# Performance work log

Measured on AMD Instinct MI355X. Metric: run time of the kernel, lower is better.

The kernel has to match this reference:

```python
import jax, jax.numpy as jnp
import numpy as np

NUM_HEADS = 16
HEAD_SIZE = 128


def _alibi_mask(seq_len: int, num_heads: int) -> jnp.ndarray:
    # slopes: num_heads > 8 branch -> 1 / 2**(i/2)
    if num_heads <= 8:
        slopes = jnp.asarray([1.0 / 2.0 ** i for i in range(num_heads)], dtype=jnp.float32)
    else:
        slopes = jnp.asarray([1.0 / 2.0 ** (i / 2.0) for i in range(num_heads)], dtype=jnp.float32)
    i = jnp.arange(seq_len)[:, None]
    j = jnp.arange(seq_len)[None, :]
    # -(i-j) on/below diagonal, -inf strictly above (causal)
    base = jnp.where(j <= i, -(i - j).astype(jnp.float32), -jnp.inf)  # [S, S]
    return slopes[:, None, None] * base  # [H, S, S]; slope * -inf = -inf


def setup_inputs() -> dict:
    key = jax.random.key(0)
    ks = jax.random.split(key, 5)
    H = 2048
    s = 0.02
    return {
        "x": jax.random.normal(ks[0], (2, 2048, H), dtype=jnp.float32),
        "qkv_w": jax.random.normal(ks[1], (H, 3 * NUM_HEADS * HEAD_SIZE), dtype=jnp.float32) * s,
        "qkv_b": jax.random.normal(ks[2], (3 * NUM_HEADS * HEAD_SIZE,), dtype=jnp.float32) * s,
        "out_w": jax.random.normal(ks[3], (NUM_HEADS * HEAD_SIZE, H), dtype=jnp.float32) * s,
        "out_b": jax.random.normal(ks[4], (H,), dtype=jnp.float32) * s,
    }


def reference(x, qkv_w, qkv_b, out_w, out_b):
    b, s, h = x.shape
    qkv = x @ qkv_w + qkv_b  # [b, s, 3*H*D]
    q, k, v = jnp.split(qkv, 3, axis=-1)

    def to_heads(t):
        return t.reshape(b, s, NUM_HEADS, HEAD_SIZE).transpose(0, 2, 1, 3)  # [b,h,s,d]

    q, k, v = to_heads(q), to_heads(k), to_heads(v)
    # NOTE: original module does NOT scale by 1/sqrt(d)
    scores = jnp.einsum("bhid,bhjd->bhij", q, k) + _alibi_mask(s, NUM_HEADS)[None]
    attn = jax.nn.softmax(scores, axis=-1)
    ctx = jnp.einsum("bhij,bhjd->bhid", attn, v)  # [b,h,s,d]
    ctx = ctx.transpose(0, 2, 1, 3).reshape(b, s, NUM_HEADS * HEAD_SIZE)
    return ctx @ out_w + out_b
```

## Files before the change

### kernel.cpp

```cpp
#include <hip/hip_runtime.h>

typedef _Float16 h8 __attribute__((ext_vector_type(8)));
typedef _Float16 h4 __attribute__((ext_vector_type(4)));
typedef float f4 __attribute__((ext_vector_type(4)));

#define MFMA16(a, b, c) __builtin_amdgcn_mfma_f32_16x16x32_f16((a), (b), (c), 0, 0, 0)
#define AS1 __attribute__((address_space(1)))
#define AS3 __attribute__((address_space(3)))

static __device__ __forceinline__ void load_lds16(const _Float16* g, _Float16* l) {
  __builtin_amdgcn_global_load_lds((const AS1 void*)g, (AS3 void*)l, 16, 0, 0);
}

__global__ __launch_bounds__(256) void cvt_f32_f16(const float* __restrict__ in,
                                                   _Float16* __restrict__ out, int n) {
  int i = (blockIdx.x * 256 + threadIdx.x) * 4;
  if (i < n) {
    const float4 v = *(const float4*)(in + i);
    h4 o;
    o[0] = (_Float16)v.x; o[1] = (_Float16)v.y; o[2] = (_Float16)v.z; o[3] = (_Float16)v.w;
    *(h4*)(out + i) = o;
  }
}

__global__ __launch_bounds__(256) void transpose_cvt(const float* __restrict__ W,
                                                     _Float16* __restrict__ Wt, int K, int N) {
  __shared__ _Float16 t[64][66];
  int n0 = blockIdx.x * 64, k0 = blockIdx.y * 64;
  int c = threadIdx.x & 63, r0 = threadIdx.x >> 6;
  for (int i = 0; i < 16; i++) {
    int r = r0 * 16 + i;
    t[r][c] = (_Float16)W[(size_t)(k0 + r) * N + n0 + c];
  }
  __syncthreads();
  for (int i = 0; i < 16; i++) {
    int r = r0 * 16 + i;
    Wt[(size_t)(n0 + r) * K + k0 + c] = t[c][r];
  }
}

template <int MODE>
__global__ __launch_bounds__(512, 2) void gemm_bt(const _Float16* __restrict__ A,
                                                  const _Float16* __restrict__ Bt,
                                                  const float* __restrict__ bias, int K,
                                                  _Float16* __restrict__ qp,
                                                  _Float16* __restrict__ kp,
                                                  _Float16* __restrict__ vtp,
                                                  float* __restrict__ outp, int N) {
  __shared__ __align__(16) _Float16 LDS[3][24576];
  const int m0 = blockIdx.y * 128, n0 = blockIdx.x * 256;
  const int tid = threadIdx.x;
  const int w = tid >> 6, lane = tid & 63, quad = lane >> 4, l16 = lane & 15;
  const int wmo = (w >> 2) * 64, wno = (w & 3) * 64;
  const int qq = lane >> 3, bb = lane & 7;
  const int lc8 = (bb ^ qq) * 8;

  const _Float16* ap0 = A + (size_t)(m0 + w * 16 + qq) * K + lc8;
  const _Float16* bp0 = Bt + (size_t)(n0 + w * 32 + qq) * K + lc8;
  const int wA = w * 1024, wB = 8192 + w * 2048;

  f4 acc[4][4] = {};
  const int nk = K >> 6;

#define STAGE(slot, koff)                               \
  {                                                     \
    const _Float16* ap = ap0 + (koff);                  \
    const _Float16* bp = bp0 + (koff);                  \
    _Float16* la = &LDS[slot][wA];                      \
    _Float16* lb = &LDS[slot][wB];                      \
    load_lds16(ap, la);                                 \
    load_lds16(ap + (size_t)8 * K, la + 512);           \
    load_lds16(bp, lb);                                 \
    load_lds16(bp + (size_t)8 * K, lb + 512);           \
    load_lds16(bp + (size_t)16 * K, lb + 1024);         \
    load_lds16(bp + (size_t)24 * K, lb + 1536);         \
  }

  STAGE(0, 0);
  STAGE(1, 64);
  asm volatile("s_waitcnt vmcnt(6)" ::: "memory");
  __builtin_amdgcn_s_barrier();

  int cb = 0, sb = 2;
  for (int t = 0; t < nk; ++t) {
    if (t + 2 < nk) STAGE(sb, (t + 2) * 64);
    sb = cb;
    const _Float16* As = &LDS[cb][0];
    const _Float16* Bs = &LDS[cb][8192];
#pragma unroll
    for (int ks = 0; ks < 2; ks++) {
      h8 af[4], bf[4];
#pragma unroll
      for (int mi = 0; mi < 4; mi++) {
        const int r = wmo + mi * 16 + l16;
        const int pc = (ks * 4 + quad) ^ (l16 & 7);
        af[mi] = *(const h8*)(&As[r * 64 + pc * 8]);
      }
#pragma unroll
      for (int ni = 0; ni < 4; ni++) {
        const int r = wno + ni * 16 + l16;
        const int pc = (ks * 4 + quad) ^ (l16 & 7);
        bf[ni] = *(const h8*)(&Bs[r * 64 + pc * 8]);
      }
      __builtin_amdgcn_s_setprio(1);
#pragma unroll
      for (int mi = 0; mi < 4; mi++)
#pragma unroll
        for (int ni = 0; ni < 4; ni++) acc[mi][ni] = MFMA16(af[mi], bf[ni], acc[mi][ni]);
      __builtin_amdgcn_s_setprio(0);
    }
    if (t + 1 < nk) {
      if (t + 2 < nk)
        asm volatile("s_waitcnt vmcnt(6)" ::: "memory");
      else
        asm volatile("s_waitcnt vmcnt(0)" ::: "memory");
      __builtin_amdgcn_s_barrier();
    }
    cb = (cb == 2) ? 0 : cb + 1;
  }
#undef STAGE

  if constexpr (MODE == 0) {
    _Float16* U = &LDS[0][0];
    const int which = n0 >> 11;
    const int bq = m0 >> 11, ms = m0 & 2047;
    const int wn_ = w & 3;
    const int grp = wn_ >> 1, cl = (wn_ & 1) * 64;
    for (int g = 0; g < 2; ++g) {
      __syncthreads();
      if (grp == g) {
        if (which == 2) {
#pragma unroll
          for (int mi = 0; mi < 4; mi++)
#pragma unroll
            for (int ni = 0; ni < 4; ni++) {
              const int d = cl + ni * 16 + l16;
              const float bv = bias[n0 + g * 128 + d];
              const int s0 = wmo + mi * 16 + quad * 4;
              h4 pack;
#pragma unroll
              for (int r = 0; r < 4; r++) pack[r] = (_Float16)(acc[mi][ni][r] + bv);
              *(h4*)(&U[d * 136 + s0]) = pack;
            }
        } else {
#pragma unroll
          for (int mi = 0; mi < 4; mi++)
#pragma unroll
            for (int ni = 0; ni < 4; ni++) {
              const int d = cl + ni * 16 + l16;
              const float bv = bias[n0 + g * 128 + d];
#pragma unroll
              for (int r = 0; r < 4; r++) {
                const int s = wmo + mi * 16 + quad * 4 + r;
                U[s * 136 + d] = (_Float16)(acc[mi][ni][r] + bv);
              }
            }
        }
      }
      __syncthreads();
      const int hh = ((n0 + g * 128) >> 7) & 15;
      const size_t hb = (size_t)bq * 16 + hh;
      if (which == 2) {
        _Float16* dst = vtp + hb * (size_t)(128 * 2048) + ms;
#pragma unroll
        for (int i = 0; i < 4; i++) {
          int f = i * 512 + tid, row = f >> 4, ch = f & 15;
          *(h8*)(dst + (size_t)row * 2048 + ch * 8) = *(h8*)(&U[row * 136 + ch * 8]);
        }
      } else {
        _Float16* dst = (which == 0 ? qp : kp) + (hb * 2048 + ms) * (size_t)128;
#pragma unroll
        for (int i = 0; i < 4; i++) {
          int f = i * 512 + tid, row = f >> 4, ch = f & 15;
          *(h8*)(dst + (size_t)row * 128 + ch * 8) = *(h8*)(&U[row * 136 + ch * 8]);
        }
      }
    }
  } else {
#pragma unroll
    for (int mi = 0; mi < 4; mi++)
#pragma unroll
      for (int ni = 0; ni < 4; ni++) {
        const int gm = m0 + wmo + mi * 16 + quad * 4;
        const int gn = n0 + wno + ni * 16 + l16;
        const float bv = bias[gn];
#pragma unroll
        for (int r = 0; r < 4; r++) outp[(size_t)(gm + r) * N + gn] = acc[mi][ni][r] + bv;
      }
  }
}

__global__ __launch_bounds__(256, 2) void attn_kernel(const _Float16* __restrict__ Q,
                                                      const _Float16* __restrict__ Kg,
                                                      const _Float16* __restrict__ Vt,
                                                      _Float16* __restrict__ ctx) {
  __shared__ _Float16 Ks[2][8192];
  __shared__ _Float16 Vs[2][8192];
  __shared__ _Float16 Vones[1088];
  __shared__ _Float16 Pl[4][16 * 68];

  const int bh = blockIdx.x, px = blockIdx.y;
  const int b = bh >> 4, h = bh & 15;
  const int tid = threadIdx.x, w = tid >> 6, lane = tid & 63, quad = lane >> 4, l16 = lane & 15;
  const size_t hbo = (size_t)bh * (2048 * 128);
  const _Float16* Qh = Q + hbo;
  const _Float16* Kh = Kg + hbo;
  const _Float16* Vh = Vt + hbo;
  const float slope = exp2f(-0.5f * (float)h);
  const float L2E = 1.44269504088896f;
  const float NEG = -3.0e38f;

  for (int i = tid; i < 1088; i += 256) Vones[i] = (_Float16)0.f;
  if (tid < 64) Vones[tid] = (_Float16)1.f;

  float cj[4];
  for (int jf = 0; jf < 4; jf++) cj[jf] = slope * (float)(jf * 16 + l16);

  const int kle = (l16 ^ quad) * 8, klo = kle ^ 32;
  const int lq = lane >> 3, vlc = ((lane & 7) ^ lq) * 8;

  for (int phase = 0; phase < 2; phase++) {
    const int t = phase ? px : 31 - px;
    const int qbase = t * 64 + w * 16;

    h8 aq[4];
#pragma unroll
    for (int t4 = 0; t4 < 4; t4++)
      aq[t4] = *(const h8*)(Qh + (size_t)(qbase + l16) * 128 + t4 * 32 + quad * 8);

    f4 o[9] = {};
    float m_i[4];
    for (int r = 0; r < 4; r++) m_i[r] = NEG;

    const int jtiles = t + 1;
    __syncthreads();
    if (w < 2) {
      const _Float16* kb = Kh + (size_t)(32 * w + quad) * 128;
      _Float16* dst = &Ks[0][w * 4096];
#pragma unroll
      for (int cc = 0; cc < 8; cc++)
        load_lds16(kb + (size_t)(4 * cc) * 128 + ((cc & 1) ? klo : kle), dst + cc * 512);
    } else {
      const _Float16* vb = Vh + (size_t)(64 * (w - 2) + lq) * 2048 + vlc;
      _Float16* dst = &Vs[0][(w - 2) * 4096];
#pragma unroll
      for (int cc = 0; cc < 8; cc++) load_lds16(vb + (size_t)(8 * cc) * 2048, dst + cc * 512);
    }

    for (int jt = 0; jt < jtiles; jt++) {
      const int j0 = jt * 64, cur = jt & 1;
      __syncthreads();
      if (jt + 1 < jtiles) {
        const int nj0 = j0 + 64, nb = cur ^ 1;
        if (w < 2) {
          const _Float16* kb = Kh + (size_t)(nj0 + 32 * w + quad) * 128;
          _Float16* dst = &Ks[nb][w * 4096];
#pragma unroll
          for (int cc = 0; cc < 8; cc++)
            load_lds16(kb + (size_t)(4 * cc) * 128 + ((cc & 1) ? klo : kle), dst + cc * 512);
        } else {
          const _Float16* vb = Vh + (size_t)(64 * (w - 2) + lq) * 2048 + nj0 + vlc;
          _Float16* dst = &Vs[nb][(w - 2) * 4096];
#pragma unroll
          for (int cc = 0; cc < 8; cc++) load_lds16(vb + (size_t)(8 * cc) * 2048, dst + cc * 512);
        }
      }
      f4 sc[4] = {};
#pragma unroll
      for (int jf = 0; jf < 4; jf++) {
        const int row = jf * 16 + l16;
#pragma unroll
        for (int t4 = 0; t4 < 4; t4++) {
          const int p = (t4 * 4 + quad) ^ (l16 & 7);
          h8 bk = *(const h8*)(&Ks[cur][row * 128 + p * 8]);
          sc[jf] = MFMA16(aq[t4], bk, sc[jf]);
        }
      }
      const float bj0 = slope * (float)j0;
#pragma unroll
      for (int jf = 0; jf < 4; jf++) {
        const float cb = bj0 + cj[jf];
#pragma unroll
        for (int r = 0; r < 4; r++) sc[jf][r] += cb;
      }
      if (jt == jtiles - 1) {
#pragma unroll
        for (int jf = 0; jf < 4; jf++) {
          const int j = j0 + jf * 16 + l16;
#pragma unroll
          for (int r = 0; r < 4; r++)
            if (j > qbase + quad * 4 + r) sc[jf][r] = NEG;
        }
      }
      float m_new[4], alpha[4];
#pragma unroll
      for (int r = 0; r < 4; r++) {
        float v = fmaxf(fmaxf(sc[0][r], sc[1][r]), fmaxf(sc[2][r], sc[3][r]));
        v = fmaxf(v, __shfl_xor(v, 1));
        v = fmaxf(v, __shfl_xor(v, 2));
        v = fmaxf(v, __shfl_xor(v, 4));
        v = fmaxf(v, __shfl_xor(v, 8));
        m_new[r] = fmaxf(m_i[r], v);
        alpha[r] = exp2f((m_i[r] - m_new[r]) * L2E);
        m_i[r] = m_new[r];
      }
#pragma unroll
      for (int jf = 0; jf < 4; jf++)
#pragma unroll
        for (int r = 0; r < 4; r++) sc[jf][r] = exp2f((sc[jf][r] - m_new[r]) * L2E);
#pragma unroll
      for (int nt = 0; nt < 9; nt++)
#pragma unroll
        for (int r = 0; r < 4; r++) o[nt][r] *= alpha[r];
#pragma unroll
      for (int jf = 0; jf < 4; jf++)
#pragma unroll
        for (int r = 0; r < 4; r++)
          Pl[w][(quad * 4 + r) * 68 + jf * 16 + l16] = (_Float16)sc[jf][r];
      asm volatile("s_waitcnt lgkmcnt(0)" ::: "memory");
      h8 ap0 = *(const h8*)(&Pl[w][l16 * 68 + quad * 8]);
      h8 ap1 = *(const h8*)(&Pl[w][l16 * 68 + 32 + quad * 8]);
#pragma unroll
      for (int nt = 0; nt < 8; nt++) {
        const int row = nt * 16 + l16;
        const int p0 = quad ^ (l16 & 7), p1 = (4 + quad) ^ (l16 & 7);
        h8 bv0 = *(const h8*)(&Vs[cur][row * 64 + p0 * 8]);
        h8 bv1 = *(const h8*)(&Vs[cur][row * 64 + p1 * 8]);
        o[nt] = MFMA16(ap0, bv0, o[nt]);
        o[nt] = MFMA16(ap1, bv1, o[nt]);
      }
      {
        h8 b0 = *(const h8*)(&Vones[l16 * 68 + quad * 8]);
        h8 b1 = *(const h8*)(&Vones[l16 * 68 + 32 + quad * 8]);
        o[8] = MFMA16(ap0, b0, o[8]);
        o[8] = MFMA16(ap1, b1, o[8]);
      }
    }

#pragma unroll
    for (int r = 0; r < 4; r++) {
      float lsum = __shfl(o[8][r], lane & 48);
      float inv = 1.0f / lsum;
      const int i = qbase + quad * 4 + r;
      const size_t row = (size_t)b * 2048 + i;
#pragma unroll
      for (int nt = 0; nt < 8; nt++)
        ctx[row * 2048 + h * 128 + nt * 16 + l16] = (_Float16)(o[nt][r] * inv);
    }
  }
}

extern "C" void kernel_launch(void* const* d_in, const int* in_sizes, int n_in, void* d_out,
                              int out_size, void* d_ws, size_t ws_size, hipStream_t stream) {
  const float* x = (const float*)d_in[0];
  const float* qkv_w = (const float*)d_in[1];
  const float* qkv_b = (const float*)d_in[2];
  const float* out_w = (const float*)d_in[3];
  const float* out_b = (const float*)d_in[4];
  float* out = (float*)d_out;

  char* ws = (char*)d_ws;
  if (ws_size < 117440512u) return;
  _Float16* xb  = (_Float16*)(ws + 0);
  _Float16* wqt = (_Float16*)(ws + 16777216);
  _Float16* wot = (_Float16*)(ws + 41943040);
  _Float16* q   = (_Float16*)(ws + 50331648);
  _Float16* k   = (_Float16*)(ws + 67108864);
  _Float16* vt  = (_Float16*)(ws + 83886080);
  _Float16* ctx = (_Float16*)(ws + 100663296);

  cvt_f32_f16<<<8192, 256, 0, stream>>>(x, xb, 8388608);
  transpose_cvt<<<dim3(96, 32), 256, 0, stream>>>(qkv_w, wqt, 2048, 6144);
  transpose_cvt<<<dim3(32, 32), 256, 0, stream>>>(out_w, wot, 2048, 2048);
  gemm_bt<0><<<dim3(24, 32), 512, 0, stream>>>(xb, wqt, qkv_b, 2048, q, k, vt, nullptr, 6144);
  attn_kernel<<<dim3(32, 16), 256, 0, stream>>>(q, k, vt, ctx);
  gemm_bt<1><<<dim3(8, 32), 512, 0, stream>>>(ctx, wot, out_b, 2048, nullptr, nullptr, nullptr,
                                              out, 2048);
}
```

Before: 393.5 us.

## Restructure GEMM mainloop into two-buffer split-phase pipeline with staggered A/B loads

```diff
diff --git a/kernel.cpp b/kernel.cpp
--- a/kernel.cpp
+++ b/kernel.cpp
@@ -40,95 +40,122 @@
 }
 
 template <int MODE>
-__global__ __launch_bounds__(512, 2) void gemm_bt(const _Float16* __restrict__ A,
-                                                  const _Float16* __restrict__ Bt,
-                                                  const float* __restrict__ bias, int K,
-                                                  _Float16* __restrict__ qp,
-                                                  _Float16* __restrict__ kp,
-                                                  _Float16* __restrict__ vtp,
-                                                  float* __restrict__ outp, int N) {
-  __shared__ __align__(16) _Float16 LDS[3][24576];
+__global__ __launch_bounds__(512, 2) void gemm_pipe(const _Float16* __restrict__ A,
+                                                    const _Float16* __restrict__ Bt,
+                                                    const float* __restrict__ bias, int K,
+                                                    _Float16* __restrict__ qp,
+                                                    _Float16* __restrict__ kp,
+                                                    _Float16* __restrict__ vtp,
+                                                    float* __restrict__ outp, int N) {
+  __shared__ __align__(16) _Float16 SH[49152];
   const int m0 = blockIdx.y * 128, n0 = blockIdx.x * 256;
   const int tid = threadIdx.x;
   const int w = tid >> 6, lane = tid & 63, quad = lane >> 4, l16 = lane & 15;
-  const int wmo = (w >> 2) * 64, wno = (w & 3) * 64;
-  const int qq = lane >> 3, bb = lane & 7;
-  const int lc8 = (bb ^ qq) * 8;
-
-  const _Float16* ap0 = A + (size_t)(m0 + w * 16 + qq) * K + lc8;
-  const _Float16* bp0 = Bt + (size_t)(n0 + w * 32 + qq) * K + lc8;
-  const int wA = w * 1024, wB = 8192 + w * 2048;
+  const int wm = (w >> 2) * 64, wn = (w & 3) * 64;
+  const int lq8 = lane >> 3, bb = lane & 7;
+  const int lc8 = (bb ^ lq8) * 8;
+
+  const _Float16* apr = A + (size_t)(m0 + w * 16 + lq8) * K + lc8;
+  const _Float16* bpr = Bt + (size_t)(n0 + w * 32 + lq8) * K + lc8;
+  const int NT = K >> 6;
 
   f4 acc[4][4] = {};
-  const int nk = K >> 6;
-
-#define STAGE(slot, koff)                               \
-  {                                                     \
-    const _Float16* ap = ap0 + (koff);                  \
-    const _Float16* bp = bp0 + (koff);                  \
-    _Float16* la = &LDS[slot][wA];                      \
-    _Float16* lb = &LDS[slot][wB];                      \
-    load_lds16(ap, la);                                 \
-    load_lds16(ap + (size_t)8 * K, la + 512);           \
-    load_lds16(bp, lb);                                 \
-    load_lds16(bp + (size_t)8 * K, lb + 512);           \
-    load_lds16(bp + (size_t)16 * K, lb + 1024);         \
-    load_lds16(bp + (size_t)24 * K, lb + 1536);         \
-  }
-
-  STAGE(0, 0);
-  STAGE(1, 64);
-  asm volatile("s_waitcnt vmcnt(6)" ::: "memory");
+
+#define STG_A(t)                                                   \
+  {                                                                \
+    _Float16* d0 = SH + ((t) & 1) * 24576 + (w * 16) * 64;         \
+    const _Float16* s0p = apr + (size_t)(t) * 64;                  \
+    load_lds16(s0p, d0);                                           \
+    load_lds16(s0p + (size_t)8 * K, d0 + 512);                     \
+  }
+#define STG_B(t)                                                   \
+  {                                                                \
+    _Float16* d0 = SH + ((t) & 1) * 24576 + 8192 + (w * 32) * 64;  \
+    const _Float16* s0p = bpr + (size_t)(t) * 64;                  \
+    load_lds16(s0p, d0);                                           \
+    load_lds16(s0p + (size_t)8 * K, d0 + 512);                     \
+    load_lds16(s0p + (size_t)16 * K, d0 + 1024);                   \
+    load_lds16(s0p + (size_t)24 * K, d0 + 1536);                   \
+  }
+
+  STG_A(0);
+  STG_B(0);
+  STG_B(1);
+  asm volatile("s_waitcnt vmcnt(4)" ::: "memory");
   __builtin_amdgcn_s_barrier();
-
-  int cb = 0, sb = 2;
-  for (int t = 0; t < nk; ++t) {
-    if (t + 2 < nk) STAGE(sb, (t + 2) * 64);
-    sb = cb;
-    const _Float16* As = &LDS[cb][0];
-    const _Float16* Bs = &LDS[cb][8192];
-#pragma unroll
-    for (int ks = 0; ks < 2; ks++) {
-      h8 af[4], bf[4];
-#pragma unroll
-      for (int mi = 0; mi < 4; mi++) {
-        const int r = wmo + mi * 16 + l16;
+  asm volatile("" ::: "memory");
+
+  for (int T = 0; T < NT; ++T) {
+    const _Float16* As = SH + (T & 1) * 24576;
+    const _Float16* Bs = As + 8192;
+    if (T + 1 < NT) STG_A(T + 1);
+    h8 bf[4][2], af[2][2];
+#pragma unroll
+    for (int ni = 0; ni < 4; ni++)
+#pragma unroll
+      for (int ks = 0; ks < 2; ks++) {
+        const int r = wn + ni * 16 + l16;
         const int pc = (ks * 4 + quad) ^ (l16 & 7);
-        af[mi] = *(const h8*)(&As[r * 64 + pc * 8]);
-      }
-#pragma unroll
-      for (int ni = 0; ni < 4; ni++) {
-        const int r = wno + ni * 16 + l16;
+        bf[ni][ks] = *(const h8*)(&Bs[r * 64 + pc * 8]);
+      }
+#pragma unroll
+    for (int mi = 0; mi < 2; mi++)
+#pragma unroll
+      for (int ks = 0; ks < 2; ks++) {
+        const int r = wm + mi * 16 + l16;
         const int pc = (ks * 4 + quad) ^ (l16 & 7);
-        bf[ni] = *(const h8*)(&Bs[r * 64 + pc * 8]);
-      }
-      __builtin_amdgcn_s_setprio(1);
-#pragma unroll
-      for (int mi = 0; mi < 4; mi++)
-#pragma unroll
-        for (int ni = 0; ni < 4; ni++) acc[mi][ni] = MFMA16(af[mi], bf[ni], acc[mi][ni]);
-      __builtin_amdgcn_s_setprio(0);
-    }
-    if (t + 1 < nk) {
-      if (t + 2 < nk)
-        asm volatile("s_waitcnt vmcnt(6)" ::: "memory");
-      else
-        asm volatile("s_waitcnt vmcnt(0)" ::: "memory");
-      __builtin_amdgcn_s_barrier();
-    }
-    cb = (cb == 2) ? 0 : cb + 1;
-  }
-#undef STAGE
+        af[mi][ks] = *(const h8*)(&As[r * 64 + pc * 8]);
+      }
+    __builtin_amdgcn_s_setprio(1);
+#pragma unroll
+    for (int ks = 0; ks < 2; ks++)
+#pragma unroll
+      for (int mi = 0; mi < 2; mi++)
+#pragma unroll
+        for (int ni = 0; ni < 4; ni++) acc[mi][ni] = MFMA16(af[mi][ks], bf[ni][ks], acc[mi][ni]);
+    __builtin_amdgcn_s_setprio(0);
+    asm volatile("" ::: "memory");
+    __builtin_amdgcn_s_barrier();
+    asm volatile("" ::: "memory");
+    if (T + 2 < NT) STG_B(T + 2);
+#pragma unroll
+    for (int mi = 0; mi < 2; mi++)
+#pragma unroll
+      for (int ks = 0; ks < 2; ks++) {
+        const int r = wm + 32 + mi * 16 + l16;
+        const int pc = (ks * 4 + quad) ^ (l16 & 7);
+        af[mi][ks] = *(const h8*)(&As[r * 64 + pc * 8]);
+      }
+    __builtin_amdgcn_s_setprio(1);
+#pragma unroll
+    for (int ks = 0; ks < 2; ks++)
+#pragma unroll
+      for (int mi = 0; mi < 2; mi++)
+#pragma unroll
+        for (int ni = 0; ni < 4; ni++)
+          acc[2 + mi][ni] = MFMA16(af[mi][ks], bf[ni][ks], acc[2 + mi][ni]);
+    __builtin_amdgcn_s_setprio(0);
+    if (T + 2 < NT)
+      asm volatile("s_waitcnt vmcnt(4)" ::: "memory");
+    else
+      asm volatile("s_waitcnt vmcnt(0)" ::: "memory");
+    __builtin_amdgcn_s_barrier();
+    asm volatile("" ::: "memory");
+  }
+#undef STG_A
+#undef STG_B
 
   if constexpr (MODE == 0) {
-    _Float16* U = &LDS[0][0];
+    __syncthreads();
+    _Float16* U = SH;
     const int which = n0 >> 11;
     const int bq = m0 >> 11, ms = m0 & 2047;
-    const int wn_ = w & 3;
-    const int grp = wn_ >> 1, cl = (wn_ & 1) * 64;
+    const int wc = w & 3;
+#pragma unroll
     for (int g = 0; g < 2; ++g) {
-      __syncthreads();
-      if (grp == g) {
+      if (g) __syncthreads();
+      if ((wc >> 1) == g) {
+        const int cl = (wc & 1) * 64;
         if (which == 2) {
 #pragma unroll
           for (int mi = 0; mi < 4; mi++)
@@ -136,7 +163,7 @@
             for (int ni = 0; ni < 4; ni++) {
               const int d = cl + ni * 16 + l16;
               const float bv = bias[n0 + g * 128 + d];
-              const int s0 = wmo + mi * 16 + quad * 4;
+              const int s0 = wm + mi * 16 + quad * 4;
               h4 pack;
 #pragma unroll
               for (int r = 0; r < 4; r++) pack[r] = (_Float16)(acc[mi][ni][r] + bv);
@@ -151,7 +178,7 @@
               const float bv = bias[n0 + g * 128 + d];
 #pragma unroll
               for (int r = 0; r < 4; r++) {
-                const int s = wmo + mi * 16 + quad * 4 + r;
+                const int s = wm + mi * 16 + quad * 4 + r;
                 U[s * 136 + d] = (_Float16)(acc[mi][ni][r] + bv);
               }
             }
@@ -181,8 +208,8 @@
     for (int mi = 0; mi < 4; mi++)
 #pragma unroll
       for (int ni = 0; ni < 4; ni++) {
-        const int gm = m0 + wmo + mi * 16 + quad * 4;
-        const int gn = n0 + wno + ni * 16 + l16;
+        const int gm = m0 + wm + mi * 16 + quad * 4;
+        const int gn = n0 + wn + ni * 16 + l16;
         const float bv = bias[gn];
 #pragma unroll
         for (int r = 0; r < 4; r++) outp[(size_t)(gm + r) * N + gn] = acc[mi][ni][r] + bv;
@@ -372,8 +399,8 @@
   cvt_f32_f16<<<8192, 256, 0, stream>>>(x, xb, 8388608);
   transpose_cvt<<<dim3(96, 32), 256, 0, stream>>>(qkv_w, wqt, 2048, 6144);
   transpose_cvt<<<dim3(32, 32), 256, 0, stream>>>(out_w, wot, 2048, 2048);
-  gemm_bt<0><<<dim3(24, 32), 512, 0, stream>>>(xb, wqt, qkv_b, 2048, q, k, vt, nullptr, 6144);
+  gemm_pipe<0><<<dim3(24, 32), 512, 0, stream>>>(xb, wqt, qkv_b, 2048, q, k, vt, nullptr, 6144);
   attn_kernel<<<dim3(32, 16), 256, 0, stream>>>(q, k, vt, ctx);
-  gemm_bt<1><<<dim3(8, 32), 512, 0, stream>>>(ctx, wot, out_b, 2048, nullptr, nullptr, nullptr,
-                                              out, 2048);
-}
+  gemm_pipe<1><<<dim3(8, 32), 512, 0, stream>>>(ctx, wot, out_b, 2048, nullptr, nullptr, nullptr,
+                                                out, 2048);
+}
```

After: 391.8 us. Within noise of the previous version (-0.5%).
